# Kernel optimization log

Hardware: AMD Instinct MI355X
Metric: run time of the kernel (lower is better)

The kernel has to match this reference:

```python
import jax, jax.numpy as jnp
import numpy as np
import math

H = 1024
L = 8  # num_limbs
B, S = 4, 2048


def _cube_vertices():
    v = np.array([[-1, -1, -1], [-1, -1, 1], [-1, 1, -1], [-1, 1, 1],
                  [1, -1, -1], [1, -1, 1], [1, 1, -1], [1, 1, 1]], dtype=np.float32)
    return jnp.asarray(v * (math.pi / 2))


def setup_inputs() -> dict:
    key = jax.random.key(0)
    ks = jax.random.split(key, 6)
    x = jax.random.normal(ks[0], (B, S, L, H), dtype=jnp.float32)
    limb_positions = _cube_vertices()  # [8,3], matches nn.Parameter init
    channel_threshold = jnp.asarray(0.3, dtype=jnp.float32)
    # route_proj: nn.Linear(H, H)
    bnd_r = 1.0 / math.sqrt(H)
    W_route = jax.random.uniform(ks[1], (H, H), jnp.float32, -bnd_r, bnd_r)
    b_route = jax.random.uniform(ks[2], (H,), jnp.float32, -bnd_r, bnd_r)
    # blend_gate[0]: nn.Linear(2H, H)
    bnd_g = 1.0 / math.sqrt(2 * H)
    W_gate = jax.random.uniform(ks[3], (H, 2 * H), jnp.float32, -bnd_g, bnd_g)
    b_gate = jax.random.uniform(ks[4], (H,), jnp.float32, -bnd_g, bnd_g)
    return {"x": x, "limb_positions": limb_positions, "channel_threshold": channel_threshold,
            "W_route": W_route, "b_route": b_route, "W_gate": W_gate, "b_gate": b_gate}


def _routing_matrix(limb_positions, channel_threshold):
    # midpoint of every (i,j) pair: [L, L, 3]
    mid = (limb_positions[:, None, :] + limb_positions[None, :, :]) * 0.5
    mx, my, mz = mid[..., 0], mid[..., 1], mid[..., 2]
    # gyroid(x,y,z) - t
    f = (jnp.sin(mx) * jnp.cos(my) + jnp.sin(my) * jnp.cos(mz)
         + jnp.sin(mz) * jnp.cos(mx)) - channel_threshold
    r = jax.nn.sigmoid(2.0 * f)
    eye = jnp.eye(L, dtype=r.dtype)
    r = jnp.where(eye > 0, 1.0, r)  # diagonal forced to 1
    r = r / (r.sum(axis=1, keepdims=True) + 1e-6)
    # torch builds this via .item() => constant w.r.t. autograd
    return jax.lax.stop_gradient(r)


def reference(x, limb_positions, channel_threshold, W_route, b_route, W_gate, b_gate):
    # x: [B, S, L, H] = stacked limb states in LIMB_NAMES order
    routing = _routing_matrix(limb_positions, channel_threshold)  # [L, L]
    projected = jnp.einsum('bsld,ed->bsle', x, W_route) + b_route  # route_proj
    routed = jnp.einsum('ij,bsjd->bsid', routing, projected)
    gate_in = jnp.concatenate([x, routed], axis=-1)  # [B,S,L,2H]
    gate = jax.nn.sigmoid(jnp.einsum('bslf,ef->bsle', gate_in, W_gate) + b_gate)
    out = gate * routed + (1.0 - gate) * x  # [B,S,L,H]
    return out
```

## Files before the change

kernel.cpp:

```cpp
#include <hip/hip_runtime.h>
#include <math.h>

#define H 1024
#define H2 2048
#define MTOK 65536

typedef __attribute__((ext_vector_type(8))) short short8;
typedef __attribute__((ext_vector_type(4))) float f32x4;

#define WS_R_OFF   0
#define WS_BS_OFF  256
#define WS_WR_OFF  4096
#define WS_WG_OFF  (4096 + 2*1024*1024)
#define WS_RT_OFF  (8ull*1024*1024)
#define WS_XB_OFF  (WS_RT_OFF + (size_t)MTOK*H*2)
#define WS_NEED_FULL (WS_XB_OFF + (size_t)MTOK*H*2)

static __device__ __forceinline__ unsigned short f2bf(float f) {
    unsigned int u = __float_as_uint(f);
    u = u + 0x7fffu + ((u >> 16) & 1u);
    return (unsigned short)(u >> 16);
}
static __device__ __forceinline__ float bf2f(unsigned short s) {
    return __uint_as_float(((unsigned int)s) << 16);
}
static __device__ __forceinline__ void gload16(const void* g, void* l) {
    __builtin_amdgcn_global_load_lds(
        (const __attribute__((address_space(1))) void*)g,
        (__attribute__((address_space(3))) void*)l, 16, 0, 0);
}

__global__ void k_routing(const float* __restrict__ lp, const float* __restrict__ thr,
                          float* __restrict__ wsR, float* __restrict__ wsBS) {
    int t = threadIdx.x;
    int i = t >> 3, j = t & 7;
    float mx = 0.5f * (lp[i*3+0] + lp[j*3+0]);
    float my = 0.5f * (lp[i*3+1] + lp[j*3+1]);
    float mz = 0.5f * (lp[i*3+2] + lp[j*3+2]);
    float f = sinf(mx)*cosf(my) + sinf(my)*cosf(mz) + sinf(mz)*cosf(mx) - thr[0];
    float r = 1.0f / (1.0f + expf(-2.0f * f));
    if (i == j) r = 1.0f;
    float s = r;
    s += __shfl_xor(s, 1, 64);
    s += __shfl_xor(s, 2, 64);
    s += __shfl_xor(s, 4, 64);
    float R = r / (s + 1e-6f);
    wsR[t] = R;
    if (j == 0) wsBS[i] = s / (s + 1e-6f);
}

__global__ void k_f32_to_bf16(const float* __restrict__ src, unsigned short* __restrict__ dst, int n4) {
    int i = blockIdx.x * blockDim.x + threadIdx.x;
    int stride = gridDim.x * blockDim.x;
    for (; i < n4; i += stride) {
        float4 v = reinterpret_cast<const float4*>(src)[i];
        ushort4 o = make_ushort4(f2bf(v.x), f2bf(v.y), f2bf(v.z), f2bf(v.w));
        reinterpret_cast<ushort4*>(dst)[i] = o;
    }
}


#define BAR()  __builtin_amdgcn_s_barrier()
#define SB0()  __builtin_amdgcn_sched_barrier(0)
#define WLG()  asm volatile("s_waitcnt lgkmcnt(0)" ::: "memory")

#define ASP(db, h) (&smem[((db)*2 + (h)) * 8192])
#define BSP(db, h) (&smem[32768 + ((db)*2 + (h)) * 8192])

#define MMQ(BF, mi, ni)                                                        \
    __builtin_amdgcn_s_setprio(1);                                             \
    _Pragma("unroll")                                                          \
    for (int kb = 0; kb < 2; ++kb)                                             \
    _Pragma("unroll")                                                          \
    for (int f = 0; f < 4; ++f)                                                \
    _Pragma("unroll")                                                          \
    for (int n = 0; n < 2; ++n)                                                \
        acc[(mi)+f][(ni)+n] = __builtin_amdgcn_mfma_f32_16x16x32_bf16(         \
            Af[f][kb], BF[n][kb], acc[(mi)+f][(ni)+n], 0, 0, 0);               \
    __builtin_amdgcn_s_setprio(0);

#define RD_A(qm)                                                               \
    _Pragma("unroll")                                                          \
    for (int f = 0; f < 4; ++f)                                                \
    _Pragma("unroll")                                                          \
    for (int kb = 0; kb < 2; ++kb) {                                           \
        const int r_ = (qm) + f*16 + lr;                                       \
        Af[f][kb] = *reinterpret_cast<const short8*>(                          \
            &ASP(d, ah)[r_*64 + (((kb*4 + kq) ^ sw) << 3)]);                   \
    }

#define RD_B(DST, qn)                                                          \
    _Pragma("unroll")                                                          \
    for (int f2 = 0; f2 < 2; ++f2)                                             \
    _Pragma("unroll")                                                          \
    for (int kb = 0; kb < 2; ++kb) {                                           \
        const int r_ = bo + (qn) + f2*16 + lr;                                 \
        DST[f2][kb] = *reinterpret_cast<const short8*>(                        \
            &BSP(d, bh)[r_*64 + (((kb*4 + kq) ^ sw) << 3)]);                   \
    }

__global__ __launch_bounds__(512, 2) void k_p1b(
    const unsigned short* __restrict__ xb,
    const unsigned short* __restrict__ Wr,
    const float* __restrict__ b_route,
    const float* __restrict__ wsR, const float* __restrict__ wsBS,
    unsigned short* __restrict__ routed)
{
    __shared__ unsigned short smem[65536];

    const int tid = threadIdx.x;
    const int l = (blockIdx.x & 7) * 128 + (blockIdx.x >> 3);
    const int bm = l >> 2, bn = l & 3;
    const int m0 = bm * 256, n0 = bn * 256;

    const int wid = tid >> 6, lane = tid & 63;
    const int ah = wid >> 2;
    const int bq = wid & 3;
    const int bh = bq >> 1;
    const int bo = (bq & 1) * 64;
    const int lr = lane & 15, kq = lane >> 4;
    const int lane8 = lane >> 3;
    const int c8s = ((lane & 7) ^ lane8) * 8;
    const int sw = lr & 7;

    f32x4 acc[8][4];
#pragma unroll
    for (int i = 0; i < 8; i++)
#pragma unroll
        for (int j = 0; j < 4; j++) acc[i][j] = (f32x4)0.0f;

#define STG_A1(db, h, t)                                                       \
    { const int _k0 = (t) * 64;                                                \
      _Pragma("unroll")                                                        \
      for (int q = 0; q < 2; ++q) {                                            \
          const int chunk = q * 8 + wid;                                       \
          gload16(xb + (size_t)(m0 + (h)*128 + chunk*8 + lane8) * H + _k0 + c8s,\
                  &ASP(db, h)[chunk * 512]);                                   \
      } }
#define STG_B1(db, h, t)                                                       \
    { const int _k0 = (t) * 64;                                                \
      _Pragma("unroll")                                                        \
      for (int q = 0; q < 2; ++q) {                                            \
          const int chunk = q * 8 + wid;                                       \
          gload16(Wr + (size_t)(n0 + (h)*128 + chunk*8 + lane8) * H + _k0 + c8s,\
                  &BSP(db, h)[chunk * 512]);                                   \
      } }

    STG_A1(0,0,0); STG_A1(0,1,0); STG_B1(0,0,0); STG_B1(0,1,0);
    STG_A1(1,0,1); STG_A1(1,1,1); STG_B1(1,0,1); STG_B1(1,1,1);
    asm volatile("s_waitcnt vmcnt(8)" ::: "memory");
    SB0();
    BAR();

    short8 Af[4][2], Bf0[2][2], Bf1[2][2];

    for (int t = 0; t < 16; ++t) {
        const int d = t & 1;
        const bool sA = (t > 0) && (t + 1 < 16);
        const bool sB = (t + 2 < 16);
        RD_A(0); RD_B(Bf0, 0);
        if (sA) { STG_A1(d^1, 0, t+1); }
        BAR(); WLG(); SB0();
        MMQ(Bf0, 0, 0);
        BAR();
        RD_B(Bf1, 32);
        if (sA) { STG_A1(d^1, 1, t+1); }
        BAR(); WLG(); SB0();
        MMQ(Bf1, 0, 2);
        BAR();
        RD_A(64);
        if (sB) { STG_B1(d, 0, t+2); }
        BAR(); WLG(); SB0();
        MMQ(Bf0, 4, 0);
        BAR();
        if (sB) { STG_B1(d, 1, t+2); }
        BAR(); SB0();
        MMQ(Bf1, 4, 2);
        if (sB)              { asm volatile("s_waitcnt vmcnt(4)" ::: "memory"); }
        else if (t + 1 < 16) { asm volatile("s_waitcnt vmcnt(0)" ::: "memory"); }
        SB0();
        BAR();
    }
#undef STG_A1
#undef STG_B1

    const int lowbit = kq & 1;
    float rc[4][8];
#pragma unroll
    for (int e = 0; e < 4; e++)
#pragma unroll
        for (int jj = 0; jj < 8; jj++) rc[e][jj] = wsR[(lowbit*4 + e)*8 + jj];
    float bsc[4];
#pragma unroll
    for (int e = 0; e < 4; e++) bsc[e] = wsBS[lowbit*4 + e];

#pragma unroll
    for (int mf = 0; mf < 8; ++mf) {
        const int lrow = ah*128 + mf*16 + kq*4;
#pragma unroll
        for (int nf = 0; nf < 4; ++nf) {
            const int lcol = bq*64 + nf*16 + lr;
            const float brv = b_route[n0 + lcol];
            float own[4], oth[4];
#pragma unroll
            for (int e = 0; e < 4; e++) {
                own[e] = acc[mf][nf][e];
                oth[e] = __shfl_xor(own[e], 16, 64);
            }
            float g8[8];
#pragma unroll
            for (int e = 0; e < 4; e++) {
                if (lowbit == 0) { g8[e] = own[e]; g8[4+e] = oth[e]; }
                else             { g8[e] = oth[e]; g8[4+e] = own[e]; }
            }
#pragma unroll
            for (int e = 0; e < 4; e++) {
                float m = 0.0f;
#pragma unroll
                for (int jj = 0; jj < 8; jj++) m += rc[e][jj] * g8[jj];
                m += bsc[e] * brv;
                smem[(lrow + e) * 256 + lcol] = f2bf(m);
            }
        }
    }
    __syncthreads();

    for (int r = wid; r < 256; r += 8) {
        const unsigned long long v =
            *reinterpret_cast<const unsigned long long*>(&smem[r*256 + lane*4]);
        *reinterpret_cast<unsigned long long*>(
            &routed[(size_t)(m0 + r) * H + n0 + lane*4]) = v;
    }
}

__global__ __launch_bounds__(512, 2) void k_p2b(
    const unsigned short* __restrict__ xb,
    const unsigned short* __restrict__ Wg,
    const float* __restrict__ b_gate,
    const unsigned short* __restrict__ routed,
    float* __restrict__ out)
{
    __shared__ unsigned short smem[65536];

    const int tid = threadIdx.x;
    const int l = (blockIdx.x & 7) * 128 + (blockIdx.x >> 3);
    const int bm = l >> 2, bn = l & 3;
    const int m0 = bm * 256, n0 = bn * 256;

    const int wid = tid >> 6, lane = tid & 63;
    const int ah = wid >> 2;
    const int bq = wid & 3, bh = bq >> 1, bo = (bq & 1) * 64;
    const int lr = lane & 15, kq = lane >> 4;
    const int lane8 = lane >> 3;
    const int c8s = ((lane & 7) ^ lane8) * 8;
    const int sw = lr & 7;

    f32x4 acc[8][4];
#pragma unroll
    for (int i = 0; i < 8; i++)
#pragma unroll
        for (int j = 0; j < 4; j++) acc[i][j] = (f32x4)0.0f;

#define STG_A2(db, h, t)                                                       \
    { const int _k0 = (t) * 64;                                                \
      const unsigned short* _sb = (_k0 < H) ? xb : routed;                     \
      const int _kk = (_k0 < H) ? _k0 : (_k0 - H);                             \
      _Pragma("unroll")                                                        \
      for (int q = 0; q < 2; ++q) {                                            \
          const int chunk = q * 8 + wid;                                       \
          gload16(_sb + (size_t)(m0 + (h)*128 + chunk*8 + lane8) * H + _kk + c8s,\
                  &ASP(db, h)[chunk * 512]);                                   \
      } }
#define STG_B2(db, h, t)                                                       \
    { const int _k0 = (t) * 64;                                                \
      _Pragma("unroll")                                                        \
      for (int q = 0; q < 2; ++q) {                                            \
          const int chunk = q * 8 + wid;                                       \
          gload16(Wg + (size_t)(n0 + (h)*128 + chunk*8 + lane8) * H2 + _k0 + c8s,\
                  &BSP(db, h)[chunk * 512]);                                   \
      } }

    STG_A2(0,0,0); STG_A2(0,1,0); STG_B2(0,0,0); STG_B2(0,1,0);
    STG_A2(1,0,1); STG_A2(1,1,1); STG_B2(1,0,1); STG_B2(1,1,1);
    asm volatile("s_waitcnt vmcnt(8)" ::: "memory");
    SB0();
    BAR();

    short8 Af[4][2], Bf0[2][2], Bf1[2][2];

    for (int t = 0; t < 32; ++t) {
        const int d = t & 1;
        const bool sA = (t > 0) && (t + 1 < 32);
        const bool sB = (t + 2 < 32);
        RD_A(0); RD_B(Bf0, 0);
        if (sA) { STG_A2(d^1, 0, t+1); }
        BAR(); WLG(); SB0();
        MMQ(Bf0, 0, 0);
        BAR();
        RD_B(Bf1, 32);
        if (sA) { STG_A2(d^1, 1, t+1); }
        BAR(); WLG(); SB0();
        MMQ(Bf1, 0, 2);
        BAR();
        RD_A(64);
        if (sB) { STG_B2(d, 0, t+2); }
        BAR(); WLG(); SB0();
        MMQ(Bf0, 4, 0);
        BAR();
        if (sB) { STG_B2(d, 1, t+2); }
        BAR(); SB0();
        MMQ(Bf1, 4, 2);
        if (sB)              { asm volatile("s_waitcnt vmcnt(4)" ::: "memory"); }
        else if (t + 1 < 32) { asm volatile("s_waitcnt vmcnt(0)" ::: "memory"); }
        SB0();
        BAR();
    }
#undef STG_A2
#undef STG_B2

#pragma unroll
    for (int mf = 0; mf < 8; ++mf) {
        const int lrow = ah*128 + mf*16 + kq*4;
#pragma unroll
        for (int nf = 0; nf < 4; ++nf) {
            const int lcol = bq*64 + nf*16 + lr;
            const float bg = b_gate[n0 + lcol];
#pragma unroll
            for (int e = 0; e < 4; e++) {
                const float tt = acc[mf][nf][e] + bg;
                const float g = 1.0f / (1.0f + expf(-tt));
                smem[(lrow + e) * 256 + lcol] = f2bf(g);
            }
        }
    }
    __syncthreads();

    for (int r = wid; r < 256; r += 8) {
        const size_t grow = (size_t)(m0 + r) * H + n0 + lane*4;
        const ushort4 gv = *reinterpret_cast<const ushort4*>(&smem[r*256 + lane*4]);
        const ushort4 rv = *reinterpret_cast<const ushort4*>(&routed[grow]);
        const ushort4 xv = *reinterpret_cast<const ushort4*>(&xb[grow]);
        float4 o;
        {
            const float g0 = bf2f(gv.x), g1 = bf2f(gv.y), g2 = bf2f(gv.z), g3 = bf2f(gv.w);
            o.x = g0 * bf2f(rv.x) + (1.0f - g0) * bf2f(xv.x);
            o.y = g1 * bf2f(rv.y) + (1.0f - g1) * bf2f(xv.y);
            o.z = g2 * bf2f(rv.z) + (1.0f - g2) * bf2f(xv.z);
            o.w = g3 * bf2f(rv.w) + (1.0f - g3) * bf2f(xv.w);
        }
        *reinterpret_cast<float4*>(&out[grow]) = o;
    }
}

__global__ __launch_bounds__(256) void k_fallback(
    const float* __restrict__ x, const float* __restrict__ Wr, const float* __restrict__ br,
    const float* __restrict__ Wg, const float* __restrict__ bg,
    const float* __restrict__ wsR, const float* __restrict__ wsBS,
    float* __restrict__ out)
{
    __shared__ float xs[8][H];
    __shared__ float rt[8][H];
    __shared__ float Rs[64];
    __shared__ float BSs[8];

    const int tid = threadIdx.x;
    const size_t base = (size_t)blockIdx.x * (8 * H);
    if (tid < 64) Rs[tid] = wsR[tid];
    if (tid < 8)  BSs[tid] = wsBS[tid];

#pragma unroll
    for (int it = 0; it < 8; ++it) {
        int s = it * 256 + tid;
        reinterpret_cast<float4*>(&xs[0][0])[s] = reinterpret_cast<const float4*>(x + base)[s];
    }
    __syncthreads();

    for (int eo = 0; eo < 4; ++eo) {
        int e = eo * 256 + tid;
        float acc[8];
#pragma unroll
        for (int l = 0; l < 8; l++) acc[l] = 0.0f;
        const float* w = Wr + (size_t)e * H;
        for (int k = 0; k < H; k += 4) {
            float4 wv = *reinterpret_cast<const float4*>(w + k);
#pragma unroll
            for (int l = 0; l < 8; l++)
                acc[l] += wv.x * xs[l][k] + wv.y * xs[l][k+1] + wv.z * xs[l][k+2] + wv.w * xs[l][k+3];
        }
        float brv = br[e];
#pragma unroll
        for (int l = 0; l < 8; l++) {
            float m = 0.0f;
#pragma unroll
            for (int j = 0; j < 8; j++) m += Rs[l*8 + j] * acc[j];
            rt[l][e] = m + BSs[l] * brv;
        }
    }
    __syncthreads();

    for (int eo = 0; eo < 4; ++eo) {
        int e = eo * 256 + tid;
        float acc2[8];
#pragma unroll
        for (int l = 0; l < 8; l++) acc2[l] = 0.0f;
        const float* w1 = Wg + (size_t)e * (2 * H);
        for (int k = 0; k < H; k += 4) {
            float4 wv = *reinterpret_cast<const float4*>(w1 + k);
#pragma unroll
            for (int l = 0; l < 8; l++)
                acc2[l] += wv.x * xs[l][k] + wv.y * xs[l][k+1] + wv.z * xs[l][k+2] + wv.w * xs[l][k+3];
        }
        const float* w2 = w1 + H;
        for (int k = 0; k < H; k += 4) {
            float4 wv = *reinterpret_cast<const float4*>(w2 + k);
#pragma unroll
            for (int l = 0; l < 8; l++)
                acc2[l] += wv.x * rt[l][k] + wv.y * rt[l][k+1] + wv.z * rt[l][k+2] + wv.w * rt[l][k+3];
        }
        float bgv = bg[e];
#pragma unroll
        for (int l = 0; l < 8; l++) {
            float t = acc2[l] + bgv;
            float g = 1.0f / (1.0f + expf(-t));
            out[base + (size_t)l * H + e] = g * rt[l][e] + (1.0f - g) * xs[l][e];
        }
    }
}

extern "C" void kernel_launch(void* const* d_in, const int* in_sizes, int n_in,
                              void* d_out, int out_size, void* d_ws, size_t ws_size,
                              hipStream_t stream) {
    const float* x   = (const float*)d_in[0];
    const float* lp  = (const float*)d_in[1];
    const float* thr = (const float*)d_in[2];
    const float* Wr  = (const float*)d_in[3];
    const float* br  = (const float*)d_in[4];
    const float* Wg  = (const float*)d_in[5];
    const float* bg  = (const float*)d_in[6];
    float* out = (float*)d_out;
    char* ws = (char*)d_ws;

    float* wsR  = (float*)(ws + WS_R_OFF);
    float* wsBS = (float*)(ws + WS_BS_OFF);

    k_routing<<<1, 64, 0, stream>>>(lp, thr, wsR, wsBS);

    if (ws_size >= WS_NEED_FULL) {
        unsigned short* wsWr = (unsigned short*)(ws + WS_WR_OFF);
        unsigned short* wsWg = (unsigned short*)(ws + WS_WG_OFF);
        unsigned short* wsRt = (unsigned short*)(ws + WS_RT_OFF);
        unsigned short* wsXb = (unsigned short*)(ws + WS_XB_OFF);
        k_f32_to_bf16<<<512, 256, 0, stream>>>(Wr, wsWr, (1024 * 1024) / 4);
        k_f32_to_bf16<<<1024, 256, 0, stream>>>(Wg, wsWg, (1024 * 2048) / 4);
        k_f32_to_bf16<<<4096, 256, 0, stream>>>(x, wsXb, (MTOK * H) / 4);
        k_p1b<<<(MTOK / 256) * (H / 256), 512, 0, stream>>>(wsXb, wsWr, br, wsR, wsBS, wsRt);
        k_p2b<<<(MTOK / 256) * (H / 256), 512, 0, stream>>>(wsXb, wsWg, bg, wsRt, out);
    } else {
        k_fallback<<<MTOK / 8, 256, 0, stream>>>(x, Wr, br, Wg, bg, wsR, wsBS, out);
    }
}
```

Measured before the change: 596.2 us.

## Fold route projection into gate weights and apply routing mix in epilogue

The gate GEMM over the concatenation of x and routed is reformulated. The routed half becomes x times a precomputed product of the gate weights and the route weights, which is stored interleaved with the x half in one concatenated weight matrix. The gate GEMM then runs with K=1024 over x only, and the 8x8 limb routing mix plus the folded bias are applied on the fp32 accumulators in the epilogue using cross-lane shuffles. This adds several small weight-prep kernels: a transpose, a conversion, a bias GEMV and a 1024x1024 GEMM. MFMA work and operand traffic stay about the same, and the fused weight product is rounded to bf16, which shifts numerics.

```diff
diff --git a/kernel.cpp b/kernel.cpp
--- a/kernel.cpp
+++ b/kernel.cpp
@@ -8,12 +8,13 @@
 typedef __attribute__((ext_vector_type(8))) short short8;
 typedef __attribute__((ext_vector_type(4))) float f32x4;
 
-#define WS_R_OFF   0
-#define WS_BS_OFF  256
-#define WS_WR_OFF  4096
-#define WS_WG_OFF  (4096 + 2*1024*1024)
-#define WS_RT_OFF  (8ull*1024*1024)
-#define WS_XB_OFF  (WS_RT_OFF + (size_t)MTOK*H*2)
+#define WS_R_OFF    0
+#define WS_BS_OFF   256
+#define WS_B2_OFF   4096
+#define WS_WR_OFF   16384
+#define WS_WCAT_OFF (16384 + 2*1024*1024)
+#define WS_RT_OFF   (8ull*1024*1024)
+#define WS_XB_OFF   (WS_RT_OFF + (size_t)MTOK*H*2)
 #define WS_NEED_FULL (WS_XB_OFF + (size_t)MTOK*H*2)
 
 static __device__ __forceinline__ unsigned short f2bf(float f) {
@@ -28,6 +29,11 @@
     __builtin_amdgcn_global_load_lds(
         (const __attribute__((address_space(1))) void*)g,
         (__attribute__((address_space(3))) void*)l, 16, 0, 0);
+}
+
+static __device__ __forceinline__ int wcat_row(int e, int h) {
+    return (e >> 7) * 256 + ((e >> 6) & 1) * 128 + ((e >> 5) & 1) * 64
+         + h * 32 + ((e >> 4) & 1) * 16 + (e & 15);
 }
 
 __global__ void k_routing(const float* __restrict__ lp, const float* __restrict__ thr,
@@ -59,6 +65,127 @@
     }
 }
 
+__global__ __launch_bounds__(256) void k_transp(const float* __restrict__ src,
+                                                unsigned short* __restrict__ dst) {
+    __shared__ unsigned short t[64][65];
+    const int bx = blockIdx.x & 15;
+    const int by = blockIdx.x >> 4;
+    const int tid = threadIdx.x;
+#pragma unroll
+    for (int q = 0; q < 16; ++q) {
+        int s = q * 256 + tid;
+        int r = s >> 6, c = s & 63;
+        t[r][c] = f2bf(src[(size_t)(by*64 + r) * H + bx*64 + c]);
+    }
+    __syncthreads();
+#pragma unroll
+    for (int q = 0; q < 16; ++q) {
+        int s = q * 256 + tid;
+        int r = s >> 6, c = s & 63;
+        dst[(size_t)(bx*64 + r) * H + by*64 + c] = t[c][r];
+    }
+}
+
+__global__ void k_cvt_wg2(const float* __restrict__ Wg, unsigned short* __restrict__ dst) {
+    const int e = blockIdx.x;
+    const int c = threadIdx.x * 4;
+    float4 v = *reinterpret_cast<const float4*>(&Wg[(size_t)e * H2 + H + c]);
+    ushort4 o = make_ushort4(f2bf(v.x), f2bf(v.y), f2bf(v.z), f2bf(v.w));
+    *reinterpret_cast<ushort4*>(&dst[(size_t)e * H + c]) = o;
+}
+
+__global__ void k_prepg1(const float* __restrict__ Wg, unsigned short* __restrict__ wcat) {
+    const int e = blockIdx.x;
+    const int c = threadIdx.x * 4;
+    float4 v = *reinterpret_cast<const float4*>(&Wg[(size_t)e * H2 + c]);
+    ushort4 o = make_ushort4(f2bf(v.x), f2bf(v.y), f2bf(v.z), f2bf(v.w));
+    *reinterpret_cast<ushort4*>(&wcat[(size_t)wcat_row(e, 0) * H + c]) = o;
+}
+
+__global__ void k_brw2(const float* __restrict__ br, const float* __restrict__ Wg,
+                       float* __restrict__ b2) {
+    const int e = blockIdx.x;
+    const int lane = threadIdx.x;
+    float s = 0.0f;
+    for (int d = lane; d < H; d += 64)
+        s += br[d] * Wg[(size_t)e * H2 + H + d];
+    s += __shfl_xor(s, 1, 64);
+    s += __shfl_xor(s, 2, 64);
+    s += __shfl_xor(s, 4, 64);
+    s += __shfl_xor(s, 8, 64);
+    s += __shfl_xor(s, 16, 64);
+    s += __shfl_xor(s, 32, 64);
+    if (lane == 0) b2[e] = s;
+}
+
+__global__ __launch_bounds__(256) void k_wc(
+    const unsigned short* __restrict__ Wg2b,
+    const unsigned short* __restrict__ WrT,
+    unsigned short* __restrict__ wcat)
+{
+    __shared__ unsigned short As[128 * 64];
+    __shared__ unsigned short Bs[128 * 64];
+
+    const int tid = threadIdx.x;
+    const int bm = blockIdx.x >> 3;
+    const int bn = blockIdx.x & 7;
+    const int m0 = bm * 128, n0 = bn * 128;
+
+    const int wid = tid >> 6, lane = tid & 63;
+    const int wm = (wid >> 1) * 64, wn = (wid & 1) * 64;
+    const int lr = lane & 15, kq = lane >> 4;
+    const int lane8 = lane >> 3;
+    const int c8s = ((lane & 7) ^ lane8) * 8;
+    const int sw = lr & 7;
+
+    f32x4 acc[4][4];
+#pragma unroll
+    for (int i = 0; i < 4; i++)
+#pragma unroll
+        for (int j = 0; j < 4; j++) acc[i][j] = (f32x4)0.0f;
+
+    for (int kt = 0; kt < H / 64; ++kt) {
+        const int k0 = kt * 64;
+#pragma unroll
+        for (int it = 0; it < 4; ++it) {
+            const int sb = it * 4 + wid;
+            const int row = sb * 8 + lane8;
+            gload16(Wg2b + (size_t)(m0 + row) * H + k0 + c8s, &As[sb * 512]);
+            gload16(WrT  + (size_t)(n0 + row) * H + k0 + c8s, &Bs[sb * 512]);
+        }
+        __syncthreads();
+#pragma unroll
+        for (int ks = 0; ks < 64; ks += 32) {
+            const int off = ((((ks >> 3) + kq) ^ sw) << 3);
+            short8 a[4], b[4];
+#pragma unroll
+            for (int i = 0; i < 4; i++)
+                a[i] = *reinterpret_cast<const short8*>(&As[(wm + i*16 + lr) * 64 + off]);
+#pragma unroll
+            for (int j = 0; j < 4; j++)
+                b[j] = *reinterpret_cast<const short8*>(&Bs[(wn + j*16 + lr) * 64 + off]);
+#pragma unroll
+            for (int i = 0; i < 4; i++)
+#pragma unroll
+                for (int j = 0; j < 4; j++)
+                    acc[i][j] = __builtin_amdgcn_mfma_f32_16x16x32_bf16(a[i], b[j], acc[i][j], 0, 0, 0);
+        }
+        __syncthreads();
+    }
+
+#pragma unroll
+    for (int i = 0; i < 4; i++) {
+        int gmBase = m0 + wm + i*16 + kq*4;
+#pragma unroll
+        for (int j2 = 0; j2 < 4; j2++) {
+            int gn = n0 + wn + j2*16 + lr;
+#pragma unroll
+            for (int e = 0; e < 4; e++)
+                wcat[(size_t)wcat_row(gmBase + e, 1) * H + gn] = f2bf(acc[i][j2][e]);
+        }
+    }
+}
+
 
 #define BAR()  __builtin_amdgcn_s_barrier()
 #define SB0()  __builtin_amdgcn_sched_barrier(0)
@@ -233,23 +360,29 @@
     }
 }
 
-__global__ __launch_bounds__(512, 2) void k_p2b(
+__global__ __launch_bounds__(512, 2) void k_p2n(
     const unsigned short* __restrict__ xb,
-    const unsigned short* __restrict__ Wg,
+    const unsigned short* __restrict__ wcat,
+    const float* __restrict__ b2,
     const float* __restrict__ b_gate,
     const unsigned short* __restrict__ routed,
+    const float* __restrict__ wsR, const float* __restrict__ wsBS,
     float* __restrict__ out)
 {
     __shared__ unsigned short smem[65536];
 
     const int tid = threadIdx.x;
-    const int l = (blockIdx.x & 7) * 128 + (blockIdx.x >> 3);
-    const int bm = l >> 2, bn = l & 3;
-    const int m0 = bm * 256, n0 = bn * 256;
+    const int l = (blockIdx.x & 7) * 256 + (blockIdx.x >> 3);
+    const int bm = l >> 3, bn = l & 7;
+    const int m0 = bm * 256;
+    const int n0B = bn * 256;
+    const int n0o = bn * 128;
 
     const int wid = tid >> 6, lane = tid & 63;
     const int ah = wid >> 2;
-    const int bq = wid & 3, bh = bq >> 1, bo = (bq & 1) * 64;
+    const int bq = wid & 3;
+    const int bh = bq >> 1;
+    const int bo = (bq & 1) * 64;
     const int lr = lane & 15, kq = lane >> 4;
     const int lane8 = lane >> 3;
     const int c8s = ((lane & 7) ^ lane8) * 8;
@@ -261,94 +394,116 @@
 #pragma unroll
         for (int j = 0; j < 4; j++) acc[i][j] = (f32x4)0.0f;
 
-#define STG_A2(db, h, t)                                                       \
-    { const int _k0 = (t) * 64;                                                \
-      const unsigned short* _sb = (_k0 < H) ? xb : routed;                     \
-      const int _kk = (_k0 < H) ? _k0 : (_k0 - H);                             \
-      _Pragma("unroll")                                                        \
-      for (int q = 0; q < 2; ++q) {                                            \
-          const int chunk = q * 8 + wid;                                       \
-          gload16(_sb + (size_t)(m0 + (h)*128 + chunk*8 + lane8) * H + _kk + c8s,\
-                  &ASP(db, h)[chunk * 512]);                                   \
-      } }
-#define STG_B2(db, h, t)                                                       \
+#define STG_A3(db, h, t)                                                       \
     { const int _k0 = (t) * 64;                                                \
       _Pragma("unroll")                                                        \
       for (int q = 0; q < 2; ++q) {                                            \
           const int chunk = q * 8 + wid;                                       \
-          gload16(Wg + (size_t)(n0 + (h)*128 + chunk*8 + lane8) * H2 + _k0 + c8s,\
+          gload16(xb + (size_t)(m0 + (h)*128 + chunk*8 + lane8) * H + _k0 + c8s,\
+                  &ASP(db, h)[chunk * 512]);                                   \
+      } }
+#define STG_B3(db, h, t)                                                       \
+    { const int _k0 = (t) * 64;                                                \
+      _Pragma("unroll")                                                        \
+      for (int q = 0; q < 2; ++q) {                                            \
+          const int chunk = q * 8 + wid;                                       \
+          gload16(wcat + (size_t)(n0B + (h)*128 + chunk*8 + lane8) * H + _k0 + c8s,\
                   &BSP(db, h)[chunk * 512]);                                   \
       } }
 
-    STG_A2(0,0,0); STG_A2(0,1,0); STG_B2(0,0,0); STG_B2(0,1,0);
-    STG_A2(1,0,1); STG_A2(1,1,1); STG_B2(1,0,1); STG_B2(1,1,1);
+    STG_A3(0,0,0); STG_A3(0,1,0); STG_B3(0,0,0); STG_B3(0,1,0);
+    STG_A3(1,0,1); STG_A3(1,1,1); STG_B3(1,0,1); STG_B3(1,1,1);
     asm volatile("s_waitcnt vmcnt(8)" ::: "memory");
     SB0();
     BAR();
 
     short8 Af[4][2], Bf0[2][2], Bf1[2][2];
 
-    for (int t = 0; t < 32; ++t) {
+    for (int t = 0; t < 16; ++t) {
         const int d = t & 1;
-        const bool sA = (t > 0) && (t + 1 < 32);
-        const bool sB = (t + 2 < 32);
+        const bool sA = (t > 0) && (t + 1 < 16);
+        const bool sB = (t + 2 < 16);
         RD_A(0); RD_B(Bf0, 0);
-        if (sA) { STG_A2(d^1, 0, t+1); }
+        if (sA) { STG_A3(d^1, 0, t+1); }
         BAR(); WLG(); SB0();
         MMQ(Bf0, 0, 0);
         BAR();
         RD_B(Bf1, 32);
-        if (sA) { STG_A2(d^1, 1, t+1); }
+        if (sA) { STG_A3(d^1, 1, t+1); }
         BAR(); WLG(); SB0();
         MMQ(Bf1, 0, 2);
         BAR();
         RD_A(64);
-        if (sB) { STG_B2(d, 0, t+2); }
+        if (sB) { STG_B3(d, 0, t+2); }
         BAR(); WLG(); SB0();
         MMQ(Bf0, 4, 0);
         BAR();
-        if (sB) { STG_B2(d, 1, t+2); }
+        if (sB) { STG_B3(d, 1, t+2); }
         BAR(); SB0();
         MMQ(Bf1, 4, 2);
         if (sB)              { asm volatile("s_waitcnt vmcnt(4)" ::: "memory"); }
-        else if (t + 1 < 32) { asm volatile("s_waitcnt vmcnt(0)" ::: "memory"); }
+        else if (t + 1 < 16) { asm volatile("s_waitcnt vmcnt(0)" ::: "memory"); }
         SB0();
         BAR();
     }
-#undef STG_A2
-#undef STG_B2
+#undef STG_A3
+#undef STG_B3
+
+    const int lowbit = kq & 1;
+    float rc[4][8];
+#pragma unroll
+    for (int e = 0; e < 4; e++)
+#pragma unroll
+        for (int jj = 0; jj < 8; jj++) rc[e][jj] = wsR[(lowbit*4 + e)*8 + jj];
+    float bsc[4];
+#pragma unroll
+    for (int e = 0; e < 4; e++) bsc[e] = wsBS[lowbit*4 + e];
 
 #pragma unroll
     for (int mf = 0; mf < 8; ++mf) {
         const int lrow = ah*128 + mf*16 + kq*4;
 #pragma unroll
-        for (int nf = 0; nf < 4; ++nf) {
-            const int lcol = bq*64 + nf*16 + lr;
-            const float bg = b_gate[n0 + lcol];
+        for (int nc = 0; nc < 2; ++nc) {
+            const int lcol = bh*64 + (bq & 1)*32 + nc*16 + lr;
+            const int gcol = n0o + lcol;
+            const float b2v = b2[gcol];
+            const float bgv = b_gate[gcol];
+            float own[4], oth[4];
 #pragma unroll
             for (int e = 0; e < 4; e++) {
-                const float tt = acc[mf][nf][e] + bg;
+                own[e] = acc[mf][nc + 2][e];
+                oth[e] = __shfl_xor(own[e], 16, 64);
+            }
+            float g8[8];
+#pragma unroll
+            for (int e = 0; e < 4; e++) {
+                if (lowbit == 0) { g8[e] = own[e]; g8[4+e] = oth[e]; }
+                else             { g8[e] = oth[e]; g8[4+e] = own[e]; }
+            }
+#pragma unroll
+            for (int e = 0; e < 4; e++) {
+                float mc = 0.0f;
+#pragma unroll
+                for (int jj = 0; jj < 8; jj++) mc += rc[e][jj] * g8[jj];
+                const float tt = acc[mf][nc][e] + mc + bsc[e]*b2v + bgv;
                 const float g = 1.0f / (1.0f + expf(-tt));
-                smem[(lrow + e) * 256 + lcol] = f2bf(g);
+                smem[(lrow + e) * 128 + lcol] = f2bf(g);
             }
         }
     }
     __syncthreads();
 
     for (int r = wid; r < 256; r += 8) {
-        const size_t grow = (size_t)(m0 + r) * H + n0 + lane*4;
-        const ushort4 gv = *reinterpret_cast<const ushort4*>(&smem[r*256 + lane*4]);
-        const ushort4 rv = *reinterpret_cast<const ushort4*>(&routed[grow]);
-        const ushort4 xv = *reinterpret_cast<const ushort4*>(&xb[grow]);
-        float4 o;
-        {
-            const float g0 = bf2f(gv.x), g1 = bf2f(gv.y), g2 = bf2f(gv.z), g3 = bf2f(gv.w);
-            o.x = g0 * bf2f(rv.x) + (1.0f - g0) * bf2f(xv.x);
-            o.y = g1 * bf2f(rv.y) + (1.0f - g1) * bf2f(xv.y);
-            o.z = g2 * bf2f(rv.z) + (1.0f - g2) * bf2f(xv.z);
-            o.w = g3 * bf2f(rv.w) + (1.0f - g3) * bf2f(xv.w);
-        }
-        *reinterpret_cast<float4*>(&out[grow]) = o;
+        const size_t grow = (size_t)(m0 + r) * H + n0o + lane*2;
+        const unsigned int g2 = *reinterpret_cast<const unsigned int*>(&smem[r*128 + lane*2]);
+        const unsigned int rv = *reinterpret_cast<const unsigned int*>(&routed[grow]);
+        const unsigned int xv = *reinterpret_cast<const unsigned int*>(&xb[grow]);
+        const float g0 = bf2f((unsigned short)(g2 & 0xffff));
+        const float g1 = bf2f((unsigned short)(g2 >> 16));
+        float2 o;
+        o.x = g0 * bf2f((unsigned short)(rv & 0xffff)) + (1.0f - g0) * bf2f((unsigned short)(xv & 0xffff));
+        o.y = g1 * bf2f((unsigned short)(rv >> 16))    + (1.0f - g1) * bf2f((unsigned short)(xv >> 16));
+        *reinterpret_cast<float2*>(&out[grow]) = o;
     }
 }
 
@@ -446,15 +601,24 @@
     k_routing<<<1, 64, 0, stream>>>(lp, thr, wsR, wsBS);
 
     if (ws_size >= WS_NEED_FULL) {
-        unsigned short* wsWr = (unsigned short*)(ws + WS_WR_OFF);
-        unsigned short* wsWg = (unsigned short*)(ws + WS_WG_OFF);
-        unsigned short* wsRt = (unsigned short*)(ws + WS_RT_OFF);
-        unsigned short* wsXb = (unsigned short*)(ws + WS_XB_OFF);
+        float* wsB2 = (float*)(ws + WS_B2_OFF);
+        unsigned short* wsWr   = (unsigned short*)(ws + WS_WR_OFF);
+        unsigned short* wsWcat = (unsigned short*)(ws + WS_WCAT_OFF);
+        unsigned short* wsRt   = (unsigned short*)(ws + WS_RT_OFF);
+        unsigned short* wsXb   = (unsigned short*)(ws + WS_XB_OFF);
+        unsigned short* scrWg2 = wsXb;
+        unsigned short* scrWrT = wsXb + 1024 * 1024;
+
         k_f32_to_bf16<<<512, 256, 0, stream>>>(Wr, wsWr, (1024 * 1024) / 4);
-        k_f32_to_bf16<<<1024, 256, 0, stream>>>(Wg, wsWg, (1024 * 2048) / 4);
+        k_transp<<<256, 256, 0, stream>>>(Wr, scrWrT);
+        k_cvt_wg2<<<1024, 256, 0, stream>>>(Wg, scrWg2);
+        k_brw2<<<1024, 64, 0, stream>>>(br, Wg, wsB2);
+        k_wc<<<64, 256, 0, stream>>>(scrWg2, scrWrT, wsWcat);
+        k_prepg1<<<1024, 256, 0, stream>>>(Wg, wsWcat);
         k_f32_to_bf16<<<4096, 256, 0, stream>>>(x, wsXb, (MTOK * H) / 4);
         k_p1b<<<(MTOK / 256) * (H / 256), 512, 0, stream>>>(wsXb, wsWr, br, wsR, wsBS, wsRt);
-        k_p2b<<<(MTOK / 256) * (H / 256), 512, 0, stream>>>(wsXb, wsWg, bg, wsRt, out);
+        k_p2n<<<(MTOK / 256) * (H2 / 256), 512, 0, stream>>>(
+            wsXb, wsWcat, wsB2, bg, wsRt, wsR, wsBS, out);
     } else {
         k_fallback<<<MTOK / 8, 256, 0, stream>>>(x, Wr, br, Wg, bg, wsR, wsBS, out);
     }
```

After: 645.2 us. 1.08x slower.
